# Kernel tuning notes

Hardware: AMD Instinct MI355X
Metric: run time of the kernel (lower is better)

## Reference

```python
import jax, jax.numpy as jnp
import numpy as np


def setup_inputs() -> dict:
    key = jax.random.key(0)
    k1, k2, k3 = jax.random.split(key, 3)
    B, S, F, K = 4096, 256, 64, 16  # batch, seq_len, n_features, n_snippets
    L = S  # snippet length == size_seq
    x = jax.random.normal(k1, (B, S, F), dtype=jnp.float32)
    W_cls = jax.random.normal(k2, (F, S, K), dtype=jnp.float32) / np.sqrt(S)
    snippet_list = jax.random.normal(k3, (F, K, L), dtype=jnp.float32)
    return {"x": x, "W_cls": W_cls, "snippet_list": snippet_list}


def reference(x, W_cls, snippet_list):
    # Replace NaNs with 0 (x[x != x] = 0 in torch)
    x = jnp.where(jnp.isnan(x), jnp.zeros_like(x), x)
    # classifier on x.transpose(2,1): [B,S,F] -> [B,F,S] -> logits [B,K,F]
    logits = jnp.einsum('bsf,fsk->bkf', x, W_cls)
    # argmax over snippet axis -> idx [B, F]
    idx = jnp.argmax(logits, axis=1)
    F = snippet_list.shape[0]
    # fused batched gather: result[b, f, :] = snippet_list[f, idx[b, f]]
    snip = snippet_list[jnp.arange(F)[None, :], idx]  # [B, F, L]
    return snip
```

## Files before the change

kernel.cpp:

```cpp
#include <hip/hip_runtime.h>
#include <stdint.h>

constexpr int Bn = 4096, Sn = 256, Fn = 64, Kn = 16;

__global__ void transpose_w_kernel(const float* __restrict__ W, float* __restrict__ Wl) {
  int t = blockIdx.x * 256 + threadIdx.x;
  int r = t & 3, f = (t >> 2) & 63, kq = (t >> 8) & 3, s = t >> 10;
  Wl[t] = W[(f * Sn + s) * Kn + kq * 4 + r];
}

__device__ __forceinline__ void gld_lds16(const float4* g, float4* l) {
  __builtin_amdgcn_global_load_lds(
      (const __attribute__((address_space(1))) uint32_t*)g,
      (__attribute__((address_space(3))) uint32_t*)l, 16, 0, 0);
}

__global__ __launch_bounds__(256, 4) void fused_kernel(
    const float* __restrict__ x, const float4* __restrict__ Wl4,
    const float4* __restrict__ snip4, float4* __restrict__ out4) {
  __shared__ float4 Wbuf[2][1024];
  __shared__ int idxs[8][64];

  const int tid = threadIdx.x;
  const int lane = tid & 63;
  const int w = tid >> 6;
  const int bbase = blockIdx.x * 8;
  const int b0 = bbase + w * 2;
  const size_t xrow = (size_t)Sn * Fn;
  const float* xb0 = x + (size_t)b0 * xrow + lane;

  float acc[2][16];
#pragma unroll
  for (int j = 0; j < 2; ++j)
#pragma unroll
    for (int k = 0; k < 16; ++k) acc[j][k] = 0.f;

  float xA[4][2], xB[4][2];

#define STAGEW(c, p)                                                         \
  {                                                                          \
    const float4* _src = Wl4 + (size_t)(c) * 1024 + w * 256 + lane;          \
    float4* _dst = &Wbuf[p][w * 256];                                        \
    _Pragma("unroll") for (int ii = 0; ii < 4; ++ii)                         \
        gld_lds16(_src + ii * 64, _dst + ii * 64);                           \
  }

#define LOADX(c, xn)                                                         \
  {                                                                          \
    _Pragma("unroll") for (int s4 = 0; s4 < 4; ++s4)                         \
        _Pragma("unroll") for (int j = 0; j < 2; ++j)                        \
            xn[s4][j] = xb0[(size_t)j * xrow + (size_t)((c) * 4 + s4) * Fn]; \
  }

#define COMPUTE(p, xn)                                                       \
  {                                                                          \
    _Pragma("unroll") for (int s4 = 0; s4 < 4; ++s4) {                       \
      float4 wq[4];                                                          \
      _Pragma("unroll") for (int kq = 0; kq < 4; ++kq)                       \
          wq[kq] = Wbuf[p][(s4 * 4 + kq) * 64 + lane];                       \
      float xv[2];                                                           \
      _Pragma("unroll") for (int j = 0; j < 2; ++j) {                        \
        float v = xn[s4][j];                                                 \
        xv[j] = (v == v) ? v : 0.f;                                          \
      }                                                                      \
      _Pragma("unroll") for (int j = 0; j < 2; ++j)                          \
          _Pragma("unroll") for (int kq = 0; kq < 4; ++kq) {                 \
        acc[j][4 * kq + 0] = fmaf(xv[j], wq[kq].x, acc[j][4 * kq + 0]);      \
        acc[j][4 * kq + 1] = fmaf(xv[j], wq[kq].y, acc[j][4 * kq + 1]);      \
        acc[j][4 * kq + 2] = fmaf(xv[j], wq[kq].z, acc[j][4 * kq + 2]);      \
        acc[j][4 * kq + 3] = fmaf(xv[j], wq[kq].w, acc[j][4 * kq + 3]);      \
      }                                                                      \
    }                                                                        \
  }

  STAGEW(0, 0);
  LOADX(0, xA);
  __syncthreads();

  for (int cc = 0; cc < 64; cc += 2) {
    STAGEW(cc + 1, 1);
    LOADX(cc + 1, xB);
    COMPUTE(0, xA);
    __syncthreads();
    if (cc + 2 < 64) {
      STAGEW(cc + 2, 0);
      LOADX(cc + 2, xA);
    }
    COMPUTE(1, xB);
    __syncthreads();
  }

#pragma unroll
  for (int j = 0; j < 2; ++j) {
    float bv = acc[j][0];
    int bk = 0;
#pragma unroll
    for (int k = 1; k < 16; ++k)
      if (acc[j][k] > bv) { bv = acc[j][k]; bk = k; }
    idxs[w * 2 + j][lane] = bk;
  }
  __syncthreads();

#pragma unroll 4
  for (int it = 0; it < 128; ++it) {
    int r = (it << 2) | w;
    int bi = r >> 6, f = r & 63;
    int kk = idxs[bi][f];
    float4 v = snip4[(size_t)((f * Kn + kk) << 6) + lane];
    out4[((size_t)(bbase + bi) * Fn + f) * 64 + lane] = v;
  }
#undef STAGEW
#undef LOADX
#undef COMPUTE
}

__global__ __launch_bounds__(256, 2) void fused_fallback(
    const float* __restrict__ x, const float* __restrict__ Wsrc,
    const float4* __restrict__ snip4, float4* __restrict__ out4) {
  __shared__ int idxs[8][64];
  const int tid = threadIdx.x;
  const int lane = tid & 63;
  const int w = tid >> 6;
  const int bbase = blockIdx.x * 8;
  const int b0 = bbase + w * 2;
  const size_t xrow = (size_t)Sn * Fn;

  float acc0[16], acc1[16];
#pragma unroll
  for (int k = 0; k < 16; ++k) { acc0[k] = 0.f; acc1[k] = 0.f; }
  const float* pc0 = x + (size_t)b0 * xrow + lane;
  const float* pc1 = pc0 + xrow;
  float xc0[8], xc1[8], xn0[8], xn1[8];
#pragma unroll
  for (int j = 0; j < 8; ++j) { xn0[j] = pc0[j * 64]; xn1[j] = pc1[j * 64]; }
  for (int c = 0; c < 32; ++c) {
#pragma unroll
    for (int j = 0; j < 8; ++j) {
      float v0 = xn0[j], v1 = xn1[j];
      xc0[j] = (v0 == v0) ? v0 : 0.f;
      xc1[j] = (v1 == v1) ? v1 : 0.f;
    }
    if (c < 31) {
      pc0 += 512; pc1 += 512;
#pragma unroll
      for (int j = 0; j < 8; ++j) { xn0[j] = pc0[j * 64]; xn1[j] = pc1[j * 64]; }
    }
#pragma unroll
    for (int s8 = 0; s8 < 8; ++s8) {
      const int s = c * 8 + s8;
      float wv[16];
      const float4* wq = reinterpret_cast<const float4*>(Wsrc) + ((size_t)(lane * Sn + s) << 2);
#pragma unroll
      for (int jj = 0; jj < 4; ++jj) {
        float4 q = wq[jj];
        wv[4 * jj + 0] = q.x; wv[4 * jj + 1] = q.y; wv[4 * jj + 2] = q.z; wv[4 * jj + 3] = q.w;
      }
#pragma unroll
      for (int k = 0; k < 16; ++k) {
        acc0[k] = fmaf(xc0[s8], wv[k], acc0[k]);
        acc1[k] = fmaf(xc1[s8], wv[k], acc1[k]);
      }
    }
  }
  {
    float bv0 = acc0[0], bv1 = acc1[0];
    int bk0 = 0, bk1 = 0;
#pragma unroll
    for (int k = 1; k < 16; ++k) {
      if (acc0[k] > bv0) { bv0 = acc0[k]; bk0 = k; }
      if (acc1[k] > bv1) { bv1 = acc1[k]; bk1 = k; }
    }
    idxs[w * 2 + 0][lane] = bk0;
    idxs[w * 2 + 1][lane] = bk1;
  }
  __syncthreads();
#pragma unroll 4
  for (int it = 0; it < 128; ++it) {
    int r = (it << 2) | w;
    int bi = r >> 6, f = r & 63;
    int kk = idxs[bi][f];
    float4 v = snip4[(size_t)((f * Kn + kk) << 6) + lane];
    out4[((size_t)(bbase + bi) * Fn + f) * 64 + lane] = v;
  }
}

extern "C" void kernel_launch(void* const* d_in, const int* in_sizes, int n_in,
                              void* d_out, int out_size, void* d_ws, size_t ws_size,
                              hipStream_t stream) {
  const float* x = (const float*)d_in[0];
  const float* W = (const float*)d_in[1];
  const float* snip = (const float*)d_in[2];
  float4* out4 = (float4*)d_out;
  const float4* snip4 = (const float4*)snip;

  const size_t wl_bytes = (size_t)Sn * Fn * Kn * sizeof(float);
  if (ws_size >= wl_bytes) {
    float* Wl = (float*)d_ws;
    transpose_w_kernel<<<(Sn * Fn * Kn) / 256, 256, 0, stream>>>(W, Wl);
    fused_kernel<<<Bn / 8, 256, 0, stream>>>(x, (const float4*)Wl, snip4, out4);
  } else {
    fused_fallback<<<Bn / 8, 256, 0, stream>>>(x, W, snip4, out4);
  }
}
```

Before: 146.1 us.

## Split sequence across wave pairs with 4 batches per wave and LDS reduction

Each wave now handles 4 batch rows over half of the sequence, not 2 rows over the whole sequence. Two wave halves each stage their own W chunk and the partial logits are summed through LDS before the argmax. This doubles reuse of each W value loaded from LDS per FMA and halves the loop trip count. In exchange it needs more registers and twice the LDS, and occupancy bounds drop from 4 to 2 blocks, so there is less latency hiding.

```diff
diff --git a/kernel.cpp b/kernel.cpp
--- a/kernel.cpp
+++ b/kernel.cpp
@@ -15,40 +15,43 @@
       (__attribute__((address_space(3))) uint32_t*)l, 16, 0, 0);
 }
 
-__global__ __launch_bounds__(256, 4) void fused_kernel(
+__global__ __launch_bounds__(256, 2) void fused_kernel(
     const float* __restrict__ x, const float4* __restrict__ Wl4,
     const float4* __restrict__ snip4, float4* __restrict__ out4) {
-  __shared__ float4 Wbuf[2][1024];
+  __shared__ float4 Wbuf[2][2][1024];
   __shared__ int idxs[8][64];
 
   const int tid = threadIdx.x;
   const int lane = tid & 63;
   const int w = tid >> 6;
+  const int q = w & 1;
+  const int h = w >> 1;
   const int bbase = blockIdx.x * 8;
-  const int b0 = bbase + w * 2;
+  const int b0 = bbase + q * 4;
   const size_t xrow = (size_t)Sn * Fn;
-  const float* xb0 = x + (size_t)b0 * xrow + lane;
-
-  float acc[2][16];
-#pragma unroll
-  for (int j = 0; j < 2; ++j)
+  const float* xb0 = x + (size_t)b0 * xrow + (size_t)(h * 128) * Fn + lane;
+  const float4* wsrc0 = Wl4 + (size_t)(h * 128) * 256;
+
+  float acc[4][16];
+#pragma unroll
+  for (int j = 0; j < 4; ++j)
 #pragma unroll
     for (int k = 0; k < 16; ++k) acc[j][k] = 0.f;
 
-  float xA[4][2], xB[4][2];
+  float xA[4][4], xB[4][4];
 
 #define STAGEW(c, p)                                                         \
   {                                                                          \
-    const float4* _src = Wl4 + (size_t)(c) * 1024 + w * 256 + lane;          \
-    float4* _dst = &Wbuf[p][w * 256];                                        \
-    _Pragma("unroll") for (int ii = 0; ii < 4; ++ii)                         \
+    const float4* _src = wsrc0 + (size_t)((c) * 4 + 2 * q) * 256 + lane;     \
+    float4* _dst = &Wbuf[h][p][(2 * q) * 256];                               \
+    _Pragma("unroll") for (int ii = 0; ii < 8; ++ii)                         \
         gld_lds16(_src + ii * 64, _dst + ii * 64);                           \
   }
 
 #define LOADX(c, xn)                                                         \
   {                                                                          \
     _Pragma("unroll") for (int s4 = 0; s4 < 4; ++s4)                         \
-        _Pragma("unroll") for (int j = 0; j < 2; ++j)                        \
+        _Pragma("unroll") for (int j = 0; j < 4; ++j)                        \
             xn[s4][j] = xb0[(size_t)j * xrow + (size_t)((c) * 4 + s4) * Fn]; \
   }
 
@@ -57,13 +60,13 @@
     _Pragma("unroll") for (int s4 = 0; s4 < 4; ++s4) {                       \
       float4 wq[4];                                                          \
       _Pragma("unroll") for (int kq = 0; kq < 4; ++kq)                       \
-          wq[kq] = Wbuf[p][(s4 * 4 + kq) * 64 + lane];                       \
-      float xv[2];                                                           \
-      _Pragma("unroll") for (int j = 0; j < 2; ++j) {                        \
+          wq[kq] = Wbuf[h][p][(s4 * 4 + kq) * 64 + lane];                    \
+      float xv[4];                                                           \
+      _Pragma("unroll") for (int j = 0; j < 4; ++j) {                        \
         float v = xn[s4][j];                                                 \
         xv[j] = (v == v) ? v : 0.f;                                          \
       }                                                                      \
-      _Pragma("unroll") for (int j = 0; j < 2; ++j)                          \
+      _Pragma("unroll") for (int j = 0; j < 4; ++j)                          \
           _Pragma("unroll") for (int kq = 0; kq < 4; ++kq) {                 \
         acc[j][4 * kq + 0] = fmaf(xv[j], wq[kq].x, acc[j][4 * kq + 0]);      \
         acc[j][4 * kq + 1] = fmaf(xv[j], wq[kq].y, acc[j][4 * kq + 1]);      \
@@ -77,12 +80,12 @@
   LOADX(0, xA);
   __syncthreads();
 
-  for (int cc = 0; cc < 64; cc += 2) {
+  for (int cc = 0; cc < 32; cc += 2) {
     STAGEW(cc + 1, 1);
     LOADX(cc + 1, xB);
     COMPUTE(0, xA);
     __syncthreads();
-    if (cc + 2 < 64) {
+    if (cc + 2 < 32) {
       STAGEW(cc + 2, 0);
       LOADX(cc + 2, xA);
     }
@@ -90,14 +93,28 @@
     __syncthreads();
   }
 
-#pragma unroll
-  for (int j = 0; j < 2; ++j) {
-    float bv = acc[j][0];
-    int bk = 0;
-#pragma unroll
-    for (int k = 1; k < 16; ++k)
-      if (acc[j][k] > bv) { bv = acc[j][k]; bk = k; }
-    idxs[w * 2 + j][lane] = bk;
+  float* red = reinterpret_cast<float*>(&Wbuf[0][0][0]);
+  if (h == 1) {
+#pragma unroll
+    for (int j = 0; j < 4; ++j)
+#pragma unroll
+      for (int k = 0; k < 16; ++k)
+        red[((q * 4 + j) * 16 + k) * 64 + lane] = acc[j][k];
+  }
+  __syncthreads();
+  if (h == 0) {
+#pragma unroll
+    for (int j = 0; j < 4; ++j) {
+#pragma unroll
+      for (int k = 0; k < 16; ++k)
+        acc[j][k] += red[((q * 4 + j) * 16 + k) * 64 + lane];
+      float bv = acc[j][0];
+      int bk = 0;
+#pragma unroll
+      for (int k = 1; k < 16; ++k)
+        if (acc[j][k] > bv) { bv = acc[j][k]; bk = k; }
+      idxs[q * 4 + j][lane] = bk;
+    }
   }
   __syncthreads();
 
@@ -152,8 +169,8 @@
       const float4* wq = reinterpret_cast<const float4*>(Wsrc) + ((size_t)(lane * Sn + s) << 2);
 #pragma unroll
       for (int jj = 0; jj < 4; ++jj) {
-        float4 q = wq[jj];
-        wv[4 * jj + 0] = q.x; wv[4 * jj + 1] = q.y; wv[4 * jj + 2] = q.z; wv[4 * jj + 3] = q.w;
+        float4 qv = wq[jj];
+        wv[4 * jj + 0] = qv.x; wv[4 * jj + 1] = qv.y; wv[4 * jj + 2] = qv.z; wv[4 * jj + 3] = qv.w;
       }
 #pragma unroll
       for (int k = 0; k < 16; ++k) {
```

Result: faster. 129.5 us (-11.4%).
